# Performance work log

Measured on AMD Instinct MI355X. Metric: run time of the kernel, lower is better.

## Reference

```python
import jax, jax.numpy as jnp
import numpy as np

DN = ('NCHW', 'OIHW', 'NCHW')
EPS = 1e-5


def _conv(x, w, b, stride, pad):
    y = jax.lax.conv_general_dilated(x, w, (stride, stride), ((pad, pad), (pad, pad)), dimension_numbers=DN)
    return y + b[None, :, None, None]


def _convT(x, w, b):
    # PyTorch ConvTranspose2d(k=4, s=2, p=1); w: (Cin, Cout, 4, 4)
    k = jnp.flip(w, (2, 3)).transpose(1, 0, 2, 3)  # -> (Cout, Cin, 4, 4)
    y = jax.lax.conv_general_dilated(x, k, (1, 1), ((2, 2), (2, 2)), lhs_dilation=(2, 2), dimension_numbers=DN)
    return y + b[None, :, None, None]


def _bn(x, g, b):
    # training-mode BatchNorm2d: batch stats over (N, H, W)
    m = x.mean((0, 2, 3), keepdims=True)
    v = x.var((0, 2, 3), keepdims=True)
    return (x - m) * jax.lax.rsqrt(v + EPS) * g[None, :, None, None] + b[None, :, None, None]


def _resblock(x, g1, b1, w3, b3, g2, b2, w1, b1c):
    h = jax.nn.relu(_bn(x, g1, b1))
    h = _conv(h, w3, b3, 1, 1)
    h = jax.nn.relu(_bn(h, g2, b2))
    h = _conv(h, w1, b1c, 1, 0)
    return h + x


def setup_inputs() -> dict:
    B, C, H, W, D, K = 16, 3, 128, 128, 256, 512
    key = jax.random.key(0)
    ks = iter(jax.random.split(key, 16))
    s = 0.05
    inp = {
        'x': jax.random.normal(next(ks), (B, C, H, W), jnp.float32),
        'ec1_w': jax.random.normal(next(ks), (D, C, 4, 4), jnp.float32) * s,
        'ec1_b': jnp.zeros((D,), jnp.float32),
        'ebn1_g': jnp.ones((D,), jnp.float32),
        'ebn1_b': jnp.zeros((D,), jnp.float32),
        'ec2_w': jax.random.normal(next(ks), (D, D, 4, 4), jnp.float32) * s,
        'ec2_b': jnp.zeros((D,), jnp.float32),
        # 4 residual blocks stacked: [0,1]=encoder, [2,3]=decoder
        'rb_bn1_g': jnp.ones((4, D), jnp.float32),
        'rb_bn1_b': jnp.zeros((4, D), jnp.float32),
        'rb_c3_w': jax.random.normal(next(ks), (4, D, D, 3, 3), jnp.float32) * s,
        'rb_c3_b': jnp.zeros((4, D), jnp.float32),
        'rb_bn2_g': jnp.ones((4, D), jnp.float32),
        'rb_bn2_b': jnp.zeros((4, D), jnp.float32),
        'rb_c1_w': jax.random.normal(next(ks), (4, D, D, 1, 1), jnp.float32) * s,
        'rb_c1_b': jnp.zeros((4, D), jnp.float32),
        'dbn1_g': jnp.ones((D,), jnp.float32),
        'dbn1_b': jnp.zeros((D,), jnp.float32),
        'dct1_w': jax.random.normal(next(ks), (D, D, 4, 4), jnp.float32) * s,  # (Cin, Cout, kH, kW)
        'dct1_b': jnp.zeros((D,), jnp.float32),
        'dbn2_g': jnp.ones((D,), jnp.float32),
        'dbn2_b': jnp.zeros((D,), jnp.float32),
        'dct2_w': jax.random.normal(next(ks), (D, C, 4, 4), jnp.float32) * s,
        'dct2_b': jnp.zeros((C,), jnp.float32),
        'codebook': jax.random.uniform(next(ks), (K, D), jnp.float32, -1.0 / K, 1.0 / K),
    }
    return inp


def reference(x, ec1_w, ec1_b, ebn1_g, ebn1_b, ec2_w, ec2_b,
              rb_bn1_g, rb_bn1_b, rb_c3_w, rb_c3_b, rb_bn2_g, rb_bn2_b, rb_c1_w, rb_c1_b,
              dbn1_g, dbn1_b, dct1_w, dct1_b, dbn2_g, dbn2_b, dct2_w, dct2_b, codebook):
    def rb(h, i):
        return _resblock(h, rb_bn1_g[i], rb_bn1_b[i], rb_c3_w[i], rb_c3_b[i],
                         rb_bn2_g[i], rb_bn2_b[i], rb_c1_w[i], rb_c1_b[i])

    # Encoder
    h = _conv(x, ec1_w, ec1_b, 2, 1)
    h = jax.nn.relu(_bn(h, ebn1_g, ebn1_b))
    h = _conv(h, ec2_w, ec2_b, 2, 1)
    h = rb(h, 0)
    z_e = rb(h, 1)  # [N, D, H/4, W/4]

    # Vector quantizer: argmin_k sum_d (z - w_k)^2 via norm expansion
    N, D, Hh, Ww = z_e.shape
    ze_f = z_e.transpose(0, 2, 3, 1).reshape(-1, D)  # [M, D]
    d2 = ((ze_f ** 2).sum(1, keepdims=True)
          - 2.0 * ze_f @ codebook.T
          + (codebook ** 2).sum(1)[None, :])  # [M, K]
    q = jnp.argmin(d2, axis=1)
    z_q = codebook[q].reshape(N, Hh, Ww, D).transpose(0, 3, 1, 2)

    # Decoder (takes z_e, per original forward)
    d = rb(z_e, 2)
    d = rb(d, 3)
    d = jax.nn.relu(_bn(d, dbn1_g, dbn1_b))
    d = _convT(d, dct1_w, dct1_b)
    d = jax.nn.relu(_bn(d, dbn2_g, dbn2_b))
    x_rec = _convT(d, dct2_w, dct2_b)

    return (x_rec, z_e, z_q)
```

## Files before the change

### kernel.cpp

```cpp
#include <hip/hip_runtime.h>
#include <stdint.h>

typedef __bf16 bf16_t;
typedef __bf16 bf16x8 __attribute__((ext_vector_type(8)));
typedef float f32x4 __attribute__((ext_vector_type(4)));

#define DEVINL __device__ __forceinline__

DEVINL float bf2f(bf16_t h){ return (float)h; }
DEVINL bf16_t f2bf(float f){ return (bf16_t)f; }

DEVINL void g2l16(const void* g, void* l){
  __builtin_amdgcn_global_load_lds(
      (const __attribute__((address_space(1))) uint32_t*)g,
      (__attribute__((address_space(3))) uint32_t*)l, 16, 0, 0);
}

#define SB_BYTES    9469952
#define SB0_OFF     35684352
#define STATS_OFF   73564160
#define CBN_OFF     73586688
#define WP_OFF      73588736
#define XI_OFF      83353600
#define WS_NEEDED   91742208
#define WP_RB3(i) (1048576 + (i)*655360)
#define WP_RB1(i) (1048576 + (i)*655360 + 589824)
#define WP_CT     3670016
#define WP_CB     4718592
#define WP_EC1    4849664
#define WP_CT2    4866048
#define WP_ELEMS  4882432

DEVINL void zerohalo_one(bf16_t* buf, int IW, int idx){
  int g8 = idx & 31, r = idx >> 5;
  int H = 4*IW - 4;
  int nn = r / H, hp = r - nn*H;
  int y, x;
  if (hp < IW){ y = 0; x = hp; }
  else if (hp < 2*IW){ y = IW-1; x = hp - IW; }
  else {
    int h2 = hp - 2*IW;
    int side = h2 / (IW-2);
    int k = h2 - side*(IW-2);
    y = k + 1; x = side ? (IW-1) : 0;
  }
  bf16_t* p = buf + ((size_t)((nn*IW + y)*IW + x))*256 + g8*8;
  bf16x8 zv;
#pragma unroll
  for (int e = 0; e < 8; e++) zv[e] = f2bf(0.f);
  *(bf16x8*)p = zv;
}

__global__ __launch_bounds__(256) void k_prep(bf16_t* __restrict__ A64, bf16_t* __restrict__ SB,
                                              uint4* __restrict__ statz){
  int b = blockIdx.x, t = threadIdx.x;
  if (b < 521){
    int idx = b*256 + t;
    if (idx < 133120) zerohalo_one(A64, 66, idx);
  } else if (b < 1577){
    int r = b - 521;
    int buf = r / 264, li = r - buf*264;
    int idx = li*256 + t;
    if (idx < 67584) zerohalo_one(SB + (size_t)buf*(SB_BYTES/2), 34, idx);
  } else {
    int i = (b - 1577)*256 + t;
    if (i < 1408) statz[i] = make_uint4(0,0,0,0);
  }
}

__global__ __launch_bounds__(256) void k_repack(
    const float* __restrict__ ec2_w, const float* __restrict__ rb_c3_w,
    const float* __restrict__ rb_c1_w, const float* __restrict__ dct1_w,
    const float* __restrict__ codebook, const float* __restrict__ ec1_w,
    const float* __restrict__ dct2_w, bf16_t* __restrict__ wp, float* __restrict__ cbn)
{
  int idx = blockIdx.x*256 + threadIdx.x;
  if (idx >= WP_ELEMS){
    int k = idx - WP_ELEMS;
    if (k < 512){
      float s = 0.f;
      for (int d = 0; d < 256; d++){ float v = codebook[k*256 + d]; s += v*v; }
      cbn[k] = s;
    }
    return;
  }
  int l = idx; float v;
  if (l < 1048576) {
    int t = l>>16, co = (l>>8)&255, ci = l&255;
    v = ec2_w[co*4096 + ci*16 + t];
  } else {
    l -= 1048576;
    if (l < 2621440) {
      int i = l / 655360;
      int r = l - i*655360;
      if (r < 589824) {
        int t = r>>16, co = (r>>8)&255, ci = r&255;
        v = rb_c3_w[i*589824 + co*2304 + ci*9 + t];
      } else {
        r -= 589824;
        int co = r>>8, ci = r&255;
        v = rb_c1_w[i*65536 + co*256 + ci];
      }
    } else {
      l -= 2621440;
      if (l < 1048576) {
        int z = l>>18, r = l&262143, t = r>>16, co = (r>>8)&255, ci = r&255;
        int py = z>>1, px = z&1, a = t>>1, b = t&1;
        int ky = 2*a + 1 - py, kx = 2*b + 1 - px;
        v = dct1_w[ci*4096 + co*16 + ky*4 + kx];
      } else {
        l -= 1048576;
        if (l < 131072) {
          v = codebook[l];
        } else {
          l -= 131072;
          if (l < 16384){
            int co = l>>6, k = l&63;
            v = (k < 48) ? ec1_w[co*48 + k] : 0.f;
          } else {
            l -= 16384;
            int n = l>>8, ci = l&255;
            v = (n < 48) ? dct2_w[ci*48 + n] : 0.f;
          }
        }
      }
    }
  }
  wp[idx] = f2bf(v);
}

__global__ __launch_bounds__(256) void k_im2col(const float* __restrict__ x, bf16_t* __restrict__ Xi){
  int m = blockIdx.x*256 + threadIdx.x;
  int nn = m >> 12, oy = (m >> 6) & 63, ox = m & 63;
  bf16_t row[64];
#pragma unroll
  for (int k = 48; k < 64; k++) row[k] = f2bf(0.f);
#pragma unroll
  for (int ci = 0; ci < 3; ci++)
#pragma unroll
    for (int ky = 0; ky < 4; ky++){
      int iy = 2*oy + ky - 1;
      bool yok = (unsigned)iy < 128u;
#pragma unroll
      for (int kx = 0; kx < 4; kx++){
        int ix = 2*ox + kx - 1;
        float v = (yok && (unsigned)ix < 128u) ? x[((size_t)((nn*3+ci)*128 + iy))*128 + ix] : 0.f;
        row[ci*16 + ky*4 + kx] = f2bf(v);
      }
    }
#pragma unroll
  for (int u = 0; u < 8; u++){
    bf16x8 o;
#pragma unroll
    for (int e = 0; e < 8; e++) o[e] = row[u*8+e];
    *(bf16x8*)(Xi + (size_t)m*64 + u*8) = o;
  }
}

__global__ __launch_bounds__(256) void k_bnapply(const bf16_t* __restrict__ in, bf16_t* __restrict__ out,
    const float* __restrict__ stat, const float* __restrict__ g, const float* __restrict__ b,
    int hwlog, float invc)
{
  int idx = blockIdx.x*256 + threadIdx.x;
  int g8 = idx & 31, p = idx >> 5;
  int HW = 1 << hwlog, IW = HW + 2;
  int xx = p & (HW-1), yy = (p >> hwlog) & (HW-1), nn = p >> (2*hwlog);
  size_t a = ((size_t)((nn*IW + yy+1)*IW + xx+1))*256 + g8*8;
  float sm[8], sq[8], gv[8], bv[8];
#pragma unroll
  for (int e = 0; e < 8; e += 4){
    *(float4*)(sm+e) = *(const float4*)(stat + g8*8 + e);
    *(float4*)(sq+e) = *(const float4*)(stat + 256 + g8*8 + e);
    *(float4*)(gv+e) = *(const float4*)(g + g8*8 + e);
    *(float4*)(bv+e) = *(const float4*)(b + g8*8 + e);
  }
  bf16x8 v = *(const bf16x8*)(in + a);
  bf16x8 o;
#pragma unroll
  for (int e = 0; e < 8; e++){
    float mean = sm[e]*invc;
    float var  = sq[e]*invc - mean*mean;
    float sc = gv[e] * rsqrtf(var + 1e-5f);
    float sh = bv[e] - mean*sc;
    o[e] = f2bf(fmaxf(bf2f(v[e])*sc + sh, 0.f));
  }
  *(bf16x8*)(out + a) = o;
}

template<int MODE>
__global__ __launch_bounds__(256) void k_gemm(
    const bf16_t* __restrict__ in, const bf16_t* __restrict__ wp,
    const float* __restrict__ bias, const bf16_t* __restrict__ res,
    bf16_t* __restrict__ outb, float* __restrict__ outf,
    float* __restrict__ stat, int out_mode, float alpha)
{
  constexpr int TAPS = (MODE==0)?16:(MODE==1)?9:(MODE==3)?4:1;
  constexpr int CHUNKS = (MODE==5)?1:TAPS*4;
  const int N = gridDim.y * 64;

  __shared__ __align__(16) bf16_t As[2][128*64];
  __shared__ __align__(16) bf16_t Bs[2][64*64];
  __shared__ float s_sum[64], s_sum2[64];

  const int tid  = threadIdx.x;
  const int lane = tid & 63;
  const int wave = tid >> 6;
  const int m0   = blockIdx.x * 128;
  const int n0   = blockIdx.y * 64;
  int ppy = 0, ppx = 0;
  const bf16_t* wpp = wp;
  if (MODE == 3){ ppy = blockIdx.z >> 1; ppx = blockIdx.z & 1; wpp += (size_t)blockIdx.z * 262144; }

  int abase[4];
#pragma unroll
  for (int j = 0; j < 4; j++){
    int s = j*256 + wave*64 + lane;
    int row = s >> 3, ug = (s & 7) ^ (row & 7);
    int m = m0 + row;
    int pbase;
    if (MODE == 0){ int nn=m>>10, sp=m&1023, oy=sp>>5, ox=sp&31; pbase = (nn*66 + 2*oy)*66 + 2*ox; }
    else if (MODE == 1){ int nn=m>>10, sp=m&1023, oy=sp>>5, ox=sp&31; pbase = (nn*34 + oy)*34 + ox; }
    else if (MODE == 3){ int nn=m>>10, sp=m&1023, oy=sp>>5, ox=sp&31; pbase = (nn*34 + oy+1+ppy)*34 + ox+1+ppx; }
    else if (MODE == 5){ pbase = 0; }
    else if (MODE == 6){ int nn=m>>12, oy=(m>>6)&63, ox=m&63; pbase = (nn*66 + oy+1)*66 + ox+1; }
    else { int nn=m>>10, sp=m&1023, oy=sp>>5, ox=sp&31; pbase = (nn*34 + oy+1)*34 + ox+1; }
    abase[j] = (MODE==5) ? (m*64 + ug*8) : (pbase*256 + ug*8);
  }
  int bbase[2];
#pragma unroll
  for (int j = 0; j < 2; j++){
    int s = j*256 + wave*64 + lane;
    int row = s >> 3, ug = (s & 7) ^ (row & 7);
    bbase[j] = (MODE==5) ? ((n0+row)*64 + ug*8) : ((n0+row)*256 + ug*8);
  }

  auto stage = [&](int buf, int c){
    int t = c >> 2;
    int koff, bko;
    if (MODE == 0){ koff = ((t>>2)*66 + (t&3))*256 + ((c&3)<<6); bko = t*65536 + ((c&3)<<6); }
    else if (MODE == 1){ int ky = t/3; koff = (ky*34 + (t - ky*3))*256 + ((c&3)<<6); bko = t*65536 + ((c&3)<<6); }
    else if (MODE == 3){ koff = -(((t>>1)*34 + (t&1))*256) + ((c&3)<<6); bko = t*65536 + ((c&3)<<6); }
    else if (MODE == 5){ koff = 0; bko = 0; }
    else { koff = (c&3)<<6; bko = (c&3)<<6; }
#pragma unroll
    for (int j = 0; j < 4; j++)
      g2l16(in + abase[j] + koff, &As[buf][(j*256 + wave*64)*8]);
#pragma unroll
    for (int j = 0; j < 2; j++)
      g2l16(wpp + bko + bbase[j], &Bs[buf][(j*256 + wave*64)*8]);
  };

  f32x4 acc[4][2];
#pragma unroll
  for (int i = 0; i < 4; i++)
#pragma unroll
    for (int j = 0; j < 2; j++) acc[i][j] = (f32x4){0.f,0.f,0.f,0.f};

  const int rowbase = (wave >> 1) * 64;
  const int colbase = (wave & 1) * 32;
  const int mf = lane & 15;
  const int kq = lane >> 4;

  stage(0, 0);
  for (int c = 0; c < CHUNKS; ++c){
    const int cur = c & 1;
    if (c + 1 < CHUNKS){
      stage(cur ^ 1, c + 1);
      asm volatile("s_waitcnt vmcnt(6)" ::: "memory");
    } else {
      asm volatile("s_waitcnt vmcnt(0)" ::: "memory");
    }
    asm volatile("s_barrier" ::: "memory");

#pragma unroll
    for (int kk = 0; kk < 2; kk++){
      bf16x8 af[4], bfr[2];
#pragma unroll
      for (int i = 0; i < 4; i++){
        int rr = rowbase + i*16 + mf;
        af[i] = *reinterpret_cast<const bf16x8*>(&As[cur][rr*64 + (((kk*4+kq) ^ (rr&7))<<3)]);
      }
#pragma unroll
      for (int j = 0; j < 2; j++){
        int rr = colbase + j*16 + mf;
        bfr[j] = *reinterpret_cast<const bf16x8*>(&Bs[cur][rr*64 + (((kk*4+kq) ^ (rr&7))<<3)]);
      }
#pragma unroll
      for (int i = 0; i < 4; i++)
#pragma unroll
        for (int j = 0; j < 2; j++)
          acc[i][j] = __builtin_amdgcn_mfma_f32_16x16x32_bf16(af[i], bfr[j], acc[i][j], 0, 0, 0);
    }
    asm volatile("s_barrier" ::: "memory");
  }

  float psum[2] = {0.f, 0.f}, psum2[2] = {0.f, 0.f};
  const int rowq = (lane >> 4) * 4;
#pragma unroll
  for (int i = 0; i < 4; i++){
#pragma unroll
    for (int r = 0; r < 4; r++){
      int m = m0 + rowbase + i*16 + rowq + r;
      int nn, oy, ox;
      if (MODE == 5 || MODE == 6){ nn = m >> 12; oy = (m >> 6) & 63; ox = m & 63; }
      else { nn = m >> 10; oy = (m >> 5) & 31; ox = m & 31; }
#pragma unroll
      for (int j = 0; j < 2; j++){
        int co = n0 + colbase + j*16 + mf;
        float v = alpha * acc[i][j][r] + (bias ? bias[co] : 0.f);
        if (res) v += bf2f(res[((size_t)((nn*34 + oy+1)*34 + ox+1))*256 + co]);
        psum[j] += v; psum2[j] += v*v;
        if (out_mode == 2){
          outf[(size_t)m * N + co] = v;
        } else if (MODE == 3){
          outb[((size_t)((nn*66 + 2*oy+ppy+1)*66 + 2*ox+ppx+1))*256 + co] = f2bf(v);
        } else if (MODE == 5){
          outb[((size_t)((nn*66 + oy+1)*66 + ox+1))*256 + co] = f2bf(v);
        } else {
          outb[((size_t)((nn*34 + oy+1)*34 + ox+1))*256 + co] = f2bf(v);
          if (out_mode == 1)
            outf[(size_t)nn*262144 + (size_t)co*1024 + oy*32 + ox] = v;
        }
      }
    }
  }
  if (stat){
    if (tid < 64){ s_sum[tid] = 0.f; s_sum2[tid] = 0.f; }
    __syncthreads();
#pragma unroll
    for (int j = 0; j < 2; j++){
      int cl = colbase + j*16 + mf;
      atomicAdd(&s_sum[cl], psum[j]);
      atomicAdd(&s_sum2[cl], psum2[j]);
    }
    __syncthreads();
    if (tid < 64){
      atomicAdd(&stat[n0 + tid], s_sum[tid]);
      atomicAdd(&stat[256 + n0 + tid], s_sum2[tid]);
    }
  }
}

__global__ __launch_bounds__(256) void k_vq_argmin(const float* __restrict__ scores,
    const float* __restrict__ cb, float* __restrict__ zq)
{
  __shared__ int best[32];
  __shared__ float Z[32*256];
  int tid = threadIdx.x, lane = tid & 63, wave = tid >> 6;
  int m0 = blockIdx.x * 32;
  int nn = m0 >> 10, y = (m0 >> 5) & 31;
  for (int rr = wave; rr < 32; rr += 4){
    const float* srow = scores + (size_t)(m0 + rr) * 512;
    float bv = 3.4e38f; int bk = 0;
    for (int k = lane; k < 512; k += 64){
      float v = srow[k];
      if (v < bv){ bv = v; bk = k; }
    }
    for (int off = 32; off; off >>= 1){
      float ov = __shfl_down(bv, off);
      int   ok = __shfl_down(bk, off);
      if (ov < bv || (ov == bv && ok < bk)){ bv = ov; bk = ok; }
    }
    if (lane == 0) best[rr] = bk;
  }
  __syncthreads();
  for (int rr = 0; rr < 32; rr++)
    Z[rr*256 + tid] = cb[best[rr]*256 + tid];
  __syncthreads();
  float* orow = zq + (size_t)nn*262144 + (size_t)tid*1024 + y*32;
#pragma unroll
  for (int x4 = 0; x4 < 8; x4++){
    float4 v;
    v.x = Z[(x4*4+0)*256 + tid];
    v.y = Z[(x4*4+1)*256 + tid];
    v.z = Z[(x4*4+2)*256 + tid];
    v.w = Z[(x4*4+3)*256 + tid];
    *(float4*)(orow + x4*4) = v;
  }
}

__global__ __launch_bounds__(256) void k_ct2asm(const float* __restrict__ P,
    const float* __restrict__ bias, float* __restrict__ out)
{
  int idx = blockIdx.x*256 + threadIdx.x;
  int nn = idx >> 14, oy2 = (idx >> 7) & 127, ox2 = idx & 127;
  int py = oy2 & 1, px = ox2 & 1, oyh = oy2 >> 1, oxh = ox2 >> 1;
  float a0 = bias[0], a1 = bias[1], a2 = bias[2];
#pragma unroll
  for (int a = 0; a < 2; a++){
    int iy = oyh + py - a;
    if ((unsigned)iy > 63u) continue;
    int ky = 2*a + 1 - py;
#pragma unroll
    for (int b = 0; b < 2; b++){
      int ix = oxh + px - b;
      if ((unsigned)ix > 63u) continue;
      int kx = 2*b + 1 - px;
      const float* pr = P + ((size_t)(nn*4096 + iy*64 + ix))*64 + ky*4 + kx;
      a0 += pr[0]; a1 += pr[16]; a2 += pr[32];
    }
  }
  size_t o = (size_t)nn*49152 + (size_t)oy2*128 + ox2;
  out[o]         = a0;
  out[o + 16384] = a1;
  out[o + 32768] = a2;
}

extern "C" void kernel_launch(void* const* d_in, const int* in_sizes, int n_in,
                              void* d_out, int out_size, void* d_ws, size_t ws_size,
                              hipStream_t stream)
{
  if (ws_size < (size_t)WS_NEEDED) return;

  const float* x       = (const float*)d_in[0];
  const float* ec1_w   = (const float*)d_in[1];
  const float* ec1_b   = (const float*)d_in[2];
  const float* ebn1_g  = (const float*)d_in[3];
  const float* ebn1_b  = (const float*)d_in[4];
  const float* ec2_w   = (const float*)d_in[5];
  const float* ec2_b   = (const float*)d_in[6];
  const float* rb_bn1_g= (const float*)d_in[7];
  const float* rb_bn1_b= (const float*)d_in[8];
  const float* rb_c3_w = (const float*)d_in[9];
  const float* rb_c3_b = (const float*)d_in[10];
  const float* rb_bn2_g= (const float*)d_in[11];
  const float* rb_bn2_b= (const float*)d_in[12];
  const float* rb_c1_w = (const float*)d_in[13];
  const float* rb_c1_b = (const float*)d_in[14];
  const float* dbn1_g  = (const float*)d_in[15];
  const float* dbn1_b  = (const float*)d_in[16];
  const float* dct1_w  = (const float*)d_in[17];
  const float* dct1_b  = (const float*)d_in[18];
  const float* dbn2_g  = (const float*)d_in[19];
  const float* dbn2_b  = (const float*)d_in[20];
  const float* dct2_w  = (const float*)d_in[21];
  const float* dct2_b  = (const float*)d_in[22];
  const float* codebook= (const float*)d_in[23];

  char* ws = (char*)d_ws;
  bf16_t* A64 = (bf16_t*)ws;
  float*  scores = (float*)ws;
  bf16_t* SB0 = (bf16_t*)(ws + SB0_OFF);
  bf16_t* SB1 = (bf16_t*)(ws + SB0_OFF + 1*SB_BYTES);
  bf16_t* SB2 = (bf16_t*)(ws + SB0_OFF + 2*SB_BYTES);
  bf16_t* SB3 = (bf16_t*)(ws + SB0_OFF + 3*SB_BYTES);
  float*  P   = (float*)(ws + SB0_OFF + 1*SB_BYTES);
  float*  stats = (float*)(ws + STATS_OFF);
  float*  cbn   = (float*)(ws + CBN_OFF);
  bf16_t* Wp    = (bf16_t*)(ws + WP_OFF);
  bf16_t* Xi    = (bf16_t*)(ws + XI_OFF);

  float* xrec = (float*)d_out;
  float* zef  = xrec + 786432;
  float* zqf  = zef + 4194304;

  k_prep  <<<dim3(1583),  256, 0, stream>>>(A64, SB0, (uint4*)(ws + STATS_OFF));
  k_repack<<<dim3(19074), 256, 0, stream>>>(ec2_w, rb_c3_w, rb_c1_w, dct1_w, codebook,
                                            ec1_w, dct2_w, Wp, cbn);

  k_im2col<<<dim3(256), 256, 0, stream>>>(x, Xi);
  k_gemm<5><<<dim3(512,4,1), 256, 0, stream>>>(Xi, Wp + WP_EC1, ec1_b, nullptr, A64, nullptr,
                                               stats, 0, 1.f);
  k_bnapply<<<dim3(8192), 256, 0, stream>>>(A64, A64, stats, ebn1_g, ebn1_b, 6, 1.f/65536.f);
  k_gemm<0><<<dim3(128,4,1), 256, 0, stream>>>(A64, Wp, ec2_b, nullptr, SB0, nullptr,
                                               stats + 1*512, 0, 1.f);

  auto launch_rb = [&](bf16_t* xin, bf16_t* xout, int i, int sIn, int sMid, int sOut, float* zf){
    k_bnapply<<<dim3(2048), 256, 0, stream>>>(xin, SB1, stats + sIn*512,
                                              rb_bn1_g + i*256, rb_bn1_b + i*256, 5, 1.f/16384.f);
    k_gemm<1><<<dim3(128,4,1), 256, 0, stream>>>(SB1, Wp + WP_RB3(i), rb_c3_b + i*256,
                                                 nullptr, SB2, nullptr, stats + sMid*512, 0, 1.f);
    k_bnapply<<<dim3(2048), 256, 0, stream>>>(SB2, SB2, stats + sMid*512,
                                              rb_bn2_g + i*256, rb_bn2_b + i*256, 5, 1.f/16384.f);
    k_gemm<2><<<dim3(128,4,1), 256, 0, stream>>>(SB2, Wp + WP_RB1(i), rb_c1_b + i*256,
                                                 xin, xout, zf, stats + sOut*512, zf ? 1 : 0, 1.f);
  };

  launch_rb(SB0, SB3, 0, 1, 2, 3, nullptr);
  launch_rb(SB3, SB0, 1, 3, 4, 5, zef);

  k_gemm<2><<<dim3(128,8,1), 256, 0, stream>>>(SB0, Wp + WP_CB, cbn, nullptr, nullptr, scores,
                                               nullptr, 2, -2.f);
  k_vq_argmin<<<dim3(512), 256, 0, stream>>>(scores, codebook, zqf);

  launch_rb(SB0, SB3, 2, 5, 6, 7, nullptr);
  launch_rb(SB3, SB0, 3, 7, 8, 9, nullptr);

  k_bnapply<<<dim3(2048), 256, 0, stream>>>(SB0, SB0, stats + 9*512, dbn1_g, dbn1_b, 5, 1.f/16384.f);
  k_gemm<3><<<dim3(128,4,4), 256, 0, stream>>>(SB0, Wp + WP_CT, dct1_b, nullptr, A64, nullptr,
                                               stats + 10*512, 0, 1.f);

  k_bnapply<<<dim3(8192), 256, 0, stream>>>(A64, A64, stats + 10*512, dbn2_g, dbn2_b, 6, 1.f/65536.f);
  k_gemm<6><<<dim3(512,1,1), 256, 0, stream>>>(A64, Wp + WP_CT2, nullptr, nullptr, nullptr, P,
                                               nullptr, 2, 1.f);
  k_ct2asm<<<dim3(1024), 256, 0, stream>>>(P, dct2_b, xrec);
}
```

Measured before the change: 738.0 us.

## Fuse BatchNorm+ReLU into GEMM A-operand loads and mask halos in-kernel

Removes every separate BN-apply kernel and instead applies the per-channel scale/shift and ReLU while loading A tiles into registers, then writing them to LDS. Padding halos are no longer zeroed in memory; out-of-bounds taps are masked to zero in-kernel, so the halo-zeroing prep work goes away and only the stats zeroing remains. This trades several full read/write passes over activations for register-staged A loads (losing async global-to-LDS for A), extra VALU work per chunk, and higher register pressure from the per-thread scale/shift tables.

New measurement: 739.8 us. No clear change (+0.2%).

```diff
diff --git a/kernel.cpp b/kernel.cpp
--- a/kernel.cpp
+++ b/kernel.cpp
@@ -31,41 +31,9 @@
 #define WP_CT2    4866048
 #define WP_ELEMS  4882432
 
-DEVINL void zerohalo_one(bf16_t* buf, int IW, int idx){
-  int g8 = idx & 31, r = idx >> 5;
-  int H = 4*IW - 4;
-  int nn = r / H, hp = r - nn*H;
-  int y, x;
-  if (hp < IW){ y = 0; x = hp; }
-  else if (hp < 2*IW){ y = IW-1; x = hp - IW; }
-  else {
-    int h2 = hp - 2*IW;
-    int side = h2 / (IW-2);
-    int k = h2 - side*(IW-2);
-    y = k + 1; x = side ? (IW-1) : 0;
-  }
-  bf16_t* p = buf + ((size_t)((nn*IW + y)*IW + x))*256 + g8*8;
-  bf16x8 zv;
-#pragma unroll
-  for (int e = 0; e < 8; e++) zv[e] = f2bf(0.f);
-  *(bf16x8*)p = zv;
-}
-
-__global__ __launch_bounds__(256) void k_prep(bf16_t* __restrict__ A64, bf16_t* __restrict__ SB,
-                                              uint4* __restrict__ statz){
-  int b = blockIdx.x, t = threadIdx.x;
-  if (b < 521){
-    int idx = b*256 + t;
-    if (idx < 133120) zerohalo_one(A64, 66, idx);
-  } else if (b < 1577){
-    int r = b - 521;
-    int buf = r / 264, li = r - buf*264;
-    int idx = li*256 + t;
-    if (idx < 67584) zerohalo_one(SB + (size_t)buf*(SB_BYTES/2), 34, idx);
-  } else {
-    int i = (b - 1577)*256 + t;
-    if (i < 1408) statz[i] = make_uint4(0,0,0,0);
-  }
+__global__ __launch_bounds__(256) void k_zero(uint4* __restrict__ p, int n16){
+  int i = blockIdx.x*256 + threadIdx.x;
+  if (i < n16) p[i] = make_uint4(0,0,0,0);
 }
 
 __global__ __launch_bounds__(256) void k_repack(
@@ -157,45 +125,18 @@
   }
 }
 
-__global__ __launch_bounds__(256) void k_bnapply(const bf16_t* __restrict__ in, bf16_t* __restrict__ out,
-    const float* __restrict__ stat, const float* __restrict__ g, const float* __restrict__ b,
-    int hwlog, float invc)
-{
-  int idx = blockIdx.x*256 + threadIdx.x;
-  int g8 = idx & 31, p = idx >> 5;
-  int HW = 1 << hwlog, IW = HW + 2;
-  int xx = p & (HW-1), yy = (p >> hwlog) & (HW-1), nn = p >> (2*hwlog);
-  size_t a = ((size_t)((nn*IW + yy+1)*IW + xx+1))*256 + g8*8;
-  float sm[8], sq[8], gv[8], bv[8];
-#pragma unroll
-  for (int e = 0; e < 8; e += 4){
-    *(float4*)(sm+e) = *(const float4*)(stat + g8*8 + e);
-    *(float4*)(sq+e) = *(const float4*)(stat + 256 + g8*8 + e);
-    *(float4*)(gv+e) = *(const float4*)(g + g8*8 + e);
-    *(float4*)(bv+e) = *(const float4*)(b + g8*8 + e);
-  }
-  bf16x8 v = *(const bf16x8*)(in + a);
-  bf16x8 o;
-#pragma unroll
-  for (int e = 0; e < 8; e++){
-    float mean = sm[e]*invc;
-    float var  = sq[e]*invc - mean*mean;
-    float sc = gv[e] * rsqrtf(var + 1e-5f);
-    float sh = bv[e] - mean*sc;
-    o[e] = f2bf(fmaxf(bf2f(v[e])*sc + sh, 0.f));
-  }
-  *(bf16x8*)(out + a) = o;
-}
-
 template<int MODE>
 __global__ __launch_bounds__(256) void k_gemm(
     const bf16_t* __restrict__ in, const bf16_t* __restrict__ wp,
     const float* __restrict__ bias, const bf16_t* __restrict__ res,
-    bf16_t* __restrict__ outb, float* __restrict__ outf,
-    float* __restrict__ stat, int out_mode, float alpha)
+    bf16_t* __restrict__ outb, float* __restrict__ outf, float* __restrict__ stat,
+    const float* __restrict__ ibn_stat, const float* __restrict__ ibn_g,
+    const float* __restrict__ ibn_b, float ibn_invc,
+    int out_mode, float alpha)
 {
   constexpr int TAPS = (MODE==0)?16:(MODE==1)?9:(MODE==3)?4:1;
   constexpr int CHUNKS = (MODE==5)?1:TAPS*4;
+  constexpr bool MASKED = (MODE==0 || MODE==1 || MODE==3);
   const int N = gridDim.y * 64;
 
   __shared__ __align__(16) bf16_t As[2][128*64];
@@ -211,21 +152,6 @@
   const bf16_t* wpp = wp;
   if (MODE == 3){ ppy = blockIdx.z >> 1; ppx = blockIdx.z & 1; wpp += (size_t)blockIdx.z * 262144; }
 
-  int abase[4];
-#pragma unroll
-  for (int j = 0; j < 4; j++){
-    int s = j*256 + wave*64 + lane;
-    int row = s >> 3, ug = (s & 7) ^ (row & 7);
-    int m = m0 + row;
-    int pbase;
-    if (MODE == 0){ int nn=m>>10, sp=m&1023, oy=sp>>5, ox=sp&31; pbase = (nn*66 + 2*oy)*66 + 2*ox; }
-    else if (MODE == 1){ int nn=m>>10, sp=m&1023, oy=sp>>5, ox=sp&31; pbase = (nn*34 + oy)*34 + ox; }
-    else if (MODE == 3){ int nn=m>>10, sp=m&1023, oy=sp>>5, ox=sp&31; pbase = (nn*34 + oy+1+ppy)*34 + ox+1+ppx; }
-    else if (MODE == 5){ pbase = 0; }
-    else if (MODE == 6){ int nn=m>>12, oy=(m>>6)&63, ox=m&63; pbase = (nn*66 + oy+1)*66 + ox+1; }
-    else { int nn=m>>10, sp=m&1023, oy=sp>>5, ox=sp&31; pbase = (nn*34 + oy+1)*34 + ox+1; }
-    abase[j] = (MODE==5) ? (m*64 + ug*8) : (pbase*256 + ug*8);
-  }
   int bbase[2];
 #pragma unroll
   for (int j = 0; j < 2; j++){
@@ -234,22 +160,6 @@
     bbase[j] = (MODE==5) ? ((n0+row)*64 + ug*8) : ((n0+row)*256 + ug*8);
   }
 
-  auto stage = [&](int buf, int c){
-    int t = c >> 2;
-    int koff, bko;
-    if (MODE == 0){ koff = ((t>>2)*66 + (t&3))*256 + ((c&3)<<6); bko = t*65536 + ((c&3)<<6); }
-    else if (MODE == 1){ int ky = t/3; koff = (ky*34 + (t - ky*3))*256 + ((c&3)<<6); bko = t*65536 + ((c&3)<<6); }
-    else if (MODE == 3){ koff = -(((t>>1)*34 + (t&1))*256) + ((c&3)<<6); bko = t*65536 + ((c&3)<<6); }
-    else if (MODE == 5){ koff = 0; bko = 0; }
-    else { koff = (c&3)<<6; bko = (c&3)<<6; }
-#pragma unroll
-    for (int j = 0; j < 4; j++)
-      g2l16(in + abase[j] + koff, &As[buf][(j*256 + wave*64)*8]);
-#pragma unroll
-    for (int j = 0; j < 2; j++)
-      g2l16(wpp + bko + bbase[j], &Bs[buf][(j*256 + wave*64)*8]);
-  };
-
   f32x4 acc[4][2];
 #pragma unroll
   for (int i = 0; i < 4; i++)
@@ -261,29 +171,34 @@
   const int mf = lane & 15;
   const int kq = lane >> 4;
 
-  stage(0, 0);
-  for (int c = 0; c < CHUNKS; ++c){
-    const int cur = c & 1;
-    if (c + 1 < CHUNKS){
-      stage(cur ^ 1, c + 1);
-      asm volatile("s_waitcnt vmcnt(6)" ::: "memory");
-    } else {
-      asm volatile("s_waitcnt vmcnt(0)" ::: "memory");
-    }
+  if constexpr (MODE == 5){
+    int abase5[4];
+#pragma unroll
+    for (int j = 0; j < 4; j++){
+      int s = j*256 + wave*64 + lane;
+      int row = s >> 3, ug = (s & 7) ^ (row & 7);
+      abase5[j] = (m0 + row)*64 + ug*8;
+    }
+#pragma unroll
+    for (int j = 0; j < 4; j++)
+      g2l16(in + abase5[j], &As[0][(j*256 + wave*64)*8]);
+#pragma unroll
+    for (int j = 0; j < 2; j++)
+      g2l16(wpp + bbase[j], &Bs[0][(j*256 + wave*64)*8]);
+    asm volatile("s_waitcnt vmcnt(0)" ::: "memory");
     asm volatile("s_barrier" ::: "memory");
-
 #pragma unroll
     for (int kk = 0; kk < 2; kk++){
       bf16x8 af[4], bfr[2];
 #pragma unroll
       for (int i = 0; i < 4; i++){
         int rr = rowbase + i*16 + mf;
-        af[i] = *reinterpret_cast<const bf16x8*>(&As[cur][rr*64 + (((kk*4+kq) ^ (rr&7))<<3)]);
+        af[i] = *reinterpret_cast<const bf16x8*>(&As[0][rr*64 + (((kk*4+kq) ^ (rr&7))<<3)]);
       }
 #pragma unroll
       for (int j = 0; j < 2; j++){
         int rr = colbase + j*16 + mf;
-        bfr[j] = *reinterpret_cast<const bf16x8*>(&Bs[cur][rr*64 + (((kk*4+kq) ^ (rr&7))<<3)]);
+        bfr[j] = *reinterpret_cast<const bf16x8*>(&Bs[0][rr*64 + (((kk*4+kq) ^ (rr&7))<<3)]);
       }
 #pragma unroll
       for (int i = 0; i < 4; i++)
@@ -291,7 +206,138 @@
         for (int j = 0; j < 2; j++)
           acc[i][j] = __builtin_amdgcn_mfma_f32_16x16x32_bf16(af[i], bfr[j], acc[i][j], 0, 0, 0);
     }
-    asm volatile("s_barrier" ::: "memory");
+  } else {
+    const int u   = tid & 7;
+    const int key = (tid >> 3) & 7;
+    int aglob[4], alds[4], aoy[4], aox[4];
+#pragma unroll
+    for (int j = 0; j < 4; j++){
+      int r = (tid >> 3) + 32*j;
+      int m = m0 + r;
+      int pbase, oy, ox, nn;
+      if (MODE == 0){ nn=m>>10; oy=(m>>5)&31; ox=m&31; pbase = (nn*66 + 2*oy)*66 + 2*ox; }
+      else if (MODE == 1){ nn=m>>10; oy=(m>>5)&31; ox=m&31; pbase = (nn*34 + oy)*34 + ox; }
+      else if (MODE == 3){ nn=m>>10; oy=(m>>5)&31; ox=m&31; pbase = (nn*34 + oy+1+ppy)*34 + ox+1+ppx; }
+      else if (MODE == 6){ nn=m>>12; oy=(m>>6)&63; ox=m&63; pbase = (nn*66 + oy+1)*66 + ox+1; }
+      else { nn=m>>10; oy=(m>>5)&31; ox=m&31; pbase = (nn*34 + oy+1)*34 + ox+1; }
+      aglob[j] = pbase*256 + u*8;
+      alds[j]  = r*64 + ((u ^ key) << 3);
+      aoy[j] = oy; aox[j] = ox;
+    }
+    const bool has_ibn = (ibn_stat != nullptr);
+    float tsc[4][8], tsh[4][8];
+    if (has_ibn){
+#pragma unroll
+      for (int p = 0; p < 4; p++){
+        int ch = p*64 + u*8;
+#pragma unroll
+        for (int e = 0; e < 8; e += 4){
+          float4 sm = *(const float4*)(ibn_stat + ch + e);
+          float4 sq = *(const float4*)(ibn_stat + 256 + ch + e);
+          float4 gg = *(const float4*)(ibn_g + ch + e);
+          float4 bb = *(const float4*)(ibn_b + ch + e);
+          float smv[4] = {sm.x,sm.y,sm.z,sm.w}, sqv[4] = {sq.x,sq.y,sq.z,sq.w};
+          float ggv[4] = {gg.x,gg.y,gg.z,gg.w}, bbv[4] = {bb.x,bb.y,bb.z,bb.w};
+#pragma unroll
+          for (int q = 0; q < 4; q++){
+            float mean = smv[q]*ibn_invc;
+            float var  = sqv[q]*ibn_invc - mean*mean;
+            float sc = ggv[q]*rsqrtf(var + 1e-5f);
+            tsc[p][e+q] = sc; tsh[p][e+q] = bbv[q] - mean*sc;
+          }
+        }
+      }
+    }
+    auto toff_of = [&](int t)->int{
+      if (MODE == 0) return ((t>>2)*66 + (t&3));
+      else if (MODE == 1){ int ky = t/3; return ky*34 + (t - ky*3); }
+      else if (MODE == 3) return -((t>>1)*34 + (t&1));
+      else return 0;
+    };
+    auto bko_of = [&](int t, int ph)->int{
+      if (MODE == 0 || MODE == 1 || MODE == 3) return t*65536 + ph*64;
+      else return ph*64;
+    };
+    bf16x8 areg[2][4];
+    auto loadA = [&](int gen, int toff, int ph){
+#pragma unroll
+      for (int j = 0; j < 4; j++)
+        areg[gen][j] = *(const bf16x8*)(in + aglob[j] + toff*256 + ph*64);
+    };
+    auto stageB = [&](int buf, int bko){
+#pragma unroll
+      for (int j = 0; j < 2; j++)
+        g2l16(wpp + bko + bbase[j], &Bs[buf][(j*256 + wave*64)*8]);
+    };
+
+    loadA(0, toff_of(0), 0);
+    stageB(0, bko_of(0, 0));
+
+    for (int c4 = 0; c4 < CHUNKS/4; ++c4){
+      bool amask[4];
+      if (MASKED){
+#pragma unroll
+        for (int j = 0; j < 4; j++){
+          int iy, ix;
+          if (MODE == 0){ iy = 2*aoy[j] + (c4>>2); ix = 2*aox[j] + (c4&3);
+                          amask[j] = (iy>=1 && iy<=64 && ix>=1 && ix<=64); }
+          else if (MODE == 1){ int ty = c4/3, tx = c4 - ty*3; iy = aoy[j]+ty; ix = aox[j]+tx;
+                          amask[j] = (iy>=1 && iy<=32 && ix>=1 && ix<=32); }
+          else { iy = aoy[j]+1+ppy-(c4>>1); ix = aox[j]+1+ppx-(c4&1);
+                          amask[j] = (iy>=1 && iy<=32 && ix>=1 && ix<=32); }
+        }
+      }
+#pragma unroll
+      for (int p = 0; p < 4; ++p){
+        const int c = c4*4 + p;
+        if (c + 1 < CHUNKS){
+          const int tn = (p==3) ? (c4+1) : c4;
+          loadA((p+1)&1, toff_of(tn), (p+1)&3);
+          stageB((p+1)&1, bko_of(tn, (p+1)&3));
+          asm volatile("s_waitcnt vmcnt(6)" ::: "memory");
+        } else {
+          asm volatile("s_waitcnt vmcnt(0)" ::: "memory");
+        }
+#pragma unroll
+        for (int j = 0; j < 4; j++){
+          bf16x8 rv = areg[p&1][j];
+          bf16x8 ov;
+          if (has_ibn){
+#pragma unroll
+            for (int e = 0; e < 8; e++){
+              float f = bf2f(rv[e])*tsc[p][e] + tsh[p][e];
+              ov[e] = f2bf(fmaxf(f, 0.f));
+            }
+          } else ov = rv;
+          if (MASKED && !amask[j]){
+#pragma unroll
+            for (int e = 0; e < 8; e++) ov[e] = f2bf(0.f);
+          }
+          *(bf16x8*)(&As[p&1][alds[j]]) = ov;
+        }
+        asm volatile("s_waitcnt lgkmcnt(0)\n\ts_barrier" ::: "memory");
+#pragma unroll
+        for (int kk = 0; kk < 2; kk++){
+          bf16x8 af[4], bfr[2];
+#pragma unroll
+          for (int i = 0; i < 4; i++){
+            int rr = rowbase + i*16 + mf;
+            af[i] = *reinterpret_cast<const bf16x8*>(&As[p&1][rr*64 + (((kk*4+kq) ^ (rr&7))<<3)]);
+          }
+#pragma unroll
+          for (int j = 0; j < 2; j++){
+            int rr = colbase + j*16 + mf;
+            bfr[j] = *reinterpret_cast<const bf16x8*>(&Bs[p&1][rr*64 + (((kk*4+kq) ^ (rr&7))<<3)]);
+          }
+#pragma unroll
+          for (int i = 0; i < 4; i++)
+#pragma unroll
+            for (int j = 0; j < 2; j++)
+              acc[i][j] = __builtin_amdgcn_mfma_f32_16x16x32_bf16(af[i], bfr[j], acc[i][j], 0, 0, 0);
+        }
+        asm volatile("s_barrier" ::: "memory");
+      }
+    }
   }
 
   float psum[2] = {0.f, 0.f}, psum2[2] = {0.f, 0.f};
@@ -441,7 +487,6 @@
   bf16_t* A64 = (bf16_t*)ws;
   float*  scores = (float*)ws;
   bf16_t* SB0 = (bf16_t*)(ws + SB0_OFF);
-  bf16_t* SB1 = (bf16_t*)(ws + SB0_OFF + 1*SB_BYTES);
   bf16_t* SB2 = (bf16_t*)(ws + SB0_OFF + 2*SB_BYTES);
   bf16_t* SB3 = (bf16_t*)(ws + SB0_OFF + 3*SB_BYTES);
   float*  P   = (float*)(ws + SB0_OFF + 1*SB_BYTES);
@@ -454,44 +499,39 @@
   float* zef  = xrec + 786432;
   float* zqf  = zef + 4194304;
 
-  k_prep  <<<dim3(1583),  256, 0, stream>>>(A64, SB0, (uint4*)(ws + STATS_OFF));
+  k_zero  <<<dim3(6),     256, 0, stream>>>((uint4*)(ws + STATS_OFF), 1408);
   k_repack<<<dim3(19074), 256, 0, stream>>>(ec2_w, rb_c3_w, rb_c1_w, dct1_w, codebook,
                                             ec1_w, dct2_w, Wp, cbn);
 
   k_im2col<<<dim3(256), 256, 0, stream>>>(x, Xi);
   k_gemm<5><<<dim3(512,4,1), 256, 0, stream>>>(Xi, Wp + WP_EC1, ec1_b, nullptr, A64, nullptr,
-                                               stats, 0, 1.f);
-  k_bnapply<<<dim3(8192), 256, 0, stream>>>(A64, A64, stats, ebn1_g, ebn1_b, 6, 1.f/65536.f);
+      stats, nullptr, nullptr, nullptr, 0.f, 0, 1.f);
   k_gemm<0><<<dim3(128,4,1), 256, 0, stream>>>(A64, Wp, ec2_b, nullptr, SB0, nullptr,
-                                               stats + 1*512, 0, 1.f);
+      stats + 1*512, stats, ebn1_g, ebn1_b, 1.f/65536.f, 0, 1.f);
 
   auto launch_rb = [&](bf16_t* xin, bf16_t* xout, int i, int sIn, int sMid, int sOut, float* zf){
-    k_bnapply<<<dim3(2048), 256, 0, stream>>>(xin, SB1, stats + sIn*512,
-                                              rb_bn1_g + i*256, rb_bn1_b + i*256, 5, 1.f/16384.f);
-    k_gemm<1><<<dim3(128,4,1), 256, 0, stream>>>(SB1, Wp + WP_RB3(i), rb_c3_b + i*256,
-                                                 nullptr, SB2, nullptr, stats + sMid*512, 0, 1.f);
-    k_bnapply<<<dim3(2048), 256, 0, stream>>>(SB2, SB2, stats + sMid*512,
-                                              rb_bn2_g + i*256, rb_bn2_b + i*256, 5, 1.f/16384.f);
+    k_gemm<1><<<dim3(128,4,1), 256, 0, stream>>>(xin, Wp + WP_RB3(i), rb_c3_b + i*256,
+        nullptr, SB2, nullptr, stats + sMid*512,
+        stats + sIn*512, rb_bn1_g + i*256, rb_bn1_b + i*256, 1.f/16384.f, 0, 1.f);
     k_gemm<2><<<dim3(128,4,1), 256, 0, stream>>>(SB2, Wp + WP_RB1(i), rb_c1_b + i*256,
-                                                 xin, xout, zf, stats + sOut*512, zf ? 1 : 0, 1.f);
+        xin, xout, zf, stats + sOut*512,
+        stats + sMid*512, rb_bn2_g + i*256, rb_bn2_b + i*256, 1.f/16384.f, zf ? 1 : 0, 1.f);
   };
 
   launch_rb(SB0, SB3, 0, 1, 2, 3, nullptr);
   launch_rb(SB3, SB0, 1, 3, 4, 5, zef);
 
   k_gemm<2><<<dim3(128,8,1), 256, 0, stream>>>(SB0, Wp + WP_CB, cbn, nullptr, nullptr, scores,
-                                               nullptr, 2, -2.f);
+      nullptr, nullptr, nullptr, nullptr, 0.f, 2, -2.f);
   k_vq_argmin<<<dim3(512), 256, 0, stream>>>(scores, codebook, zqf);
 
   launch_rb(SB0, SB3, 2, 5, 6, 7, nullptr);
   launch_rb(SB3, SB0, 3, 7, 8, 9, nullptr);
 
-  k_bnapply<<<dim3(2048), 256, 0, stream>>>(SB0, SB0, stats + 9*512, dbn1_g, dbn1_b, 5, 1.f/16384.f);
   k_gemm<3><<<dim3(128,4,4), 256, 0, stream>>>(SB0, Wp + WP_CT, dct1_b, nullptr, A64, nullptr,
-                                               stats + 10*512, 0, 1.f);
-
-  k_bnapply<<<dim3(8192), 256, 0, stream>>>(A64, A64, stats + 10*512, dbn2_g, dbn2_b, 6, 1.f/65536.f);
+      stats + 10*512, stats + 9*512, dbn1_g, dbn1_b, 1.f/16384.f, 0, 1.f);
+
   k_gemm<6><<<dim3(512,1,1), 256, 0, stream>>>(A64, Wp + WP_CT2, nullptr, nullptr, nullptr, P,
-                                               nullptr, 2, 1.f);
+      nullptr, stats + 10*512, dbn2_g, dbn2_b, 1.f/65536.f, 2, 1.f);
   k_ct2asm<<<dim3(1024), 256, 0, stream>>>(P, dct2_b, xrec);
 }
```
